# Kernel optimization log

Hardware: AMD Instinct MI355X
Metric: run time of the kernel (lower is better)

Reference implementation:

```python
import jax, jax.numpy as jnp
import numpy as np

MUL_IN = 32      # multiplicity of input 0e irrep (input channels)
MUL_OUT = 32     # multiplicity of each output irrep
NUM_RB = 8       # num_radial_basis
DIAMETER = 5.0
STEPS = (1.0, 1.0, 1.0)
GRID = 32
BATCH = 2
OUT_DIM = MUL_OUT * (1 + 3 + 5)  # 32x0e + 32x1o + 32x2e = 288


def _sus(x):
    # smooth unit step used by e3nn's 'smooth_finite' basis
    return jnp.where(x > 0.0, jnp.exp(-1.0 / jnp.where(x > 0.0, x, 1.0)), 0.0)


def _soft_one_hot(x, start, end, number):
    # e3nn.soft_one_hot_linspace, basis='smooth_finite', start_zero=end_zero=True
    values = jnp.linspace(start, end, number + 2)
    step = values[1] - values[0]
    values = values[1:-1]
    d = (x[..., None] - values) / step
    return 1.14136 * jnp.exp(2.0) * _sus(d + 1.0) * _sus(1.0 - d)


def _lattice():
    r = DIAMETER / 2
    axes = []
    for st in STEPS:
        s = int(np.floor(r / st))
        axes.append(jnp.arange(-s, s + 1.0, dtype=jnp.float32) * st)
    return jnp.stack(jnp.meshgrid(*axes, indexing='ij'), axis=-1)  # [X,Y,Z,3]


def _sph(lattice):
    # e3nn real spherical harmonics (component normalization, normalize=True),
    # e3nn axis/order convention: l=1 -> (y, z, x)
    n = jnp.linalg.norm(lattice, axis=-1, keepdims=True)
    u = lattice / jnp.where(n == 0.0, 1.0, n)
    x, y, z = u[..., 0], u[..., 1], u[..., 2]
    y0 = jnp.ones_like(x)[..., None]
    y1 = jnp.sqrt(3.0) * jnp.stack([y, z, x], axis=-1)
    y2 = jnp.stack([
        jnp.sqrt(15.0) * x * y,
        jnp.sqrt(15.0) * y * z,
        (jnp.sqrt(5.0) / 2.0) * (2.0 * z**2 - x**2 - y**2),
        jnp.sqrt(15.0) * x * z,
        (jnp.sqrt(15.0) / 2.0) * (x**2 - y**2),
    ], axis=-1)
    return [y0, y1, y2]


def _kernel(w0, w1, w2, w_lin):
    lat = _lattice()
    nvox = lat.shape[0] * lat.shape[1] * lat.shape[2]
    emb = _soft_one_hot(jnp.linalg.norm(lat, axis=-1), 0.0, DIAMETER / 2, NUM_RB)
    ys = _sph(lat)
    fan = jnp.sqrt(jnp.asarray(MUL_IN, emb.dtype))  # fully-connected TP path norm
    blocks = []
    for w, y in zip((w0, w1, w2), ys):
        # radial weights per (in-mul u, out-mul v): [X,Y,Z,u,v]
        W = jnp.einsum('xyzk,kuv->xyzuv', emb, w) / nvox
        # scalar-input TP path 0e x l -> l reduces to outer product with Y_lm
        blk = jnp.einsum('xyzuv,xyzm->xyzuvm', W, y) / fan
        blocks.append(blk.reshape(blk.shape[:4] + (-1,)))  # flatten (v, m)
    k = jnp.concatenate(blocks, axis=-1)  # [X,Y,Z,MUL_IN,OUT_DIM]
    # self-connection (FunctionalLinear) replaces the center tap; only 0e->0e path
    center = jnp.concatenate(
        [w_lin / fan, jnp.zeros((MUL_IN, MUL_OUT * (3 + 5)), k.dtype)], axis=-1)
    cx, cy, cz = k.shape[0] // 2, k.shape[1] // 2, k.shape[2] // 2
    return k.at[cx, cy, cz].set(center)


def setup_inputs() -> dict:
    key = jax.random.key(0)
    ks = jax.random.split(key, 5)
    return {
        'x': jax.random.normal(ks[0], (BATCH, GRID, GRID, GRID, MUL_IN), jnp.float32),
        'w0': jax.random.normal(ks[1], (NUM_RB, MUL_IN, MUL_OUT), jnp.float32),
        'w1': jax.random.normal(ks[2], (NUM_RB, MUL_IN, MUL_OUT), jnp.float32),
        'w2': jax.random.normal(ks[3], (NUM_RB, MUL_IN, MUL_OUT), jnp.float32),
        'w_lin': jax.random.normal(ks[4], (MUL_IN, MUL_OUT), jnp.float32),
    }


def reference(x, w0, w1, w2, w_lin):
    k = _kernel(w0, w1, w2, w_lin)  # [5,5,5,32,288]
    return jax.lax.conv_general_dilated(
        x, k, window_strides=(1, 1, 1), padding='SAME',
        dimension_numbers=('NXYZC', 'XYZIO', 'NXYZC'))
```

## Files before the change

kernel.cpp:

```cpp
#include <hip/hip_runtime.h>

typedef __bf16 bf16x8 __attribute__((ext_vector_type(8)));
typedef float f32x4 __attribute__((ext_vector_type(4)));

#define KT_BYTES 2304000
#define NS 18432
#define NV 84

__device__ __forceinline__ unsigned short f2bf(float f) {
    unsigned int u = __builtin_bit_cast(unsigned int, f);
    unsigned int r = (u + 0x7fffu + ((u >> 16) & 1u)) >> 16;
    return (unsigned short)r;
}

__device__ __forceinline__ float sus(float x) {
    return x > 0.0f ? expf(-1.0f / x) : 0.0f;
}

struct VoxTab { int kt[NV]; int xb[NV]; };
constexpr VoxTab mk_tab() {
    VoxTab t{};
    int n = 0;
    for (int dx = 0; dx < 5; dx++)
        for (int dy = 0; dy < 5; dy++)
            for (int dz = 0; dz < 5; dz++) {
                int a = dx - 2, b = dy - 2, c = dz - 2;
                if (a * a + b * b + c * c <= 6) {
                    t.kt[n] = (dx * 25 + dy * 5 + dz) * NS;
                    t.xb[n] = ((dx * 36 + dy) * 36 + dz) * 32;
                    n++;
                }
            }
    for (; n < NV; n++) { t.kt[n] = 0; t.xb[n] = 0; }
    return t;
}
__constant__ VoxTab TAB = mk_tab();

__global__ __launch_bounds__(512) void build_kt(const float* __restrict__ w0,
                                                const float* __restrict__ w1,
                                                const float* __restrict__ w2,
                                                const float* __restrict__ wlin,
                                                unsigned short* __restrict__ kt) {
    __shared__ float lw[24576];
    const int tid = threadIdx.x;
    {
        const float4* s0 = (const float4*)w0;
        const float4* s1 = (const float4*)w1;
        const float4* s2 = (const float4*)w2;
        for (int u = tid; u < 6144; u += 512) {
            int wsel = u >> 11, r = u & 2047;
            float4 v = (wsel == 0 ? s0[r] : (wsel == 1 ? s1[r] : s2[r]));
            ((float4*)lw)[u] = v;
        }
    }
    __syncthreads();

    const int v = blockIdx.x;
    const int dx = v / 25, dy = (v / 5) % 5, dz = v % 5;
    const float lx = (float)(dx - 2), ly = (float)(dy - 2), lz = (float)(dz - 2);
    const float nr = sqrtf(lx * lx + ly * ly + lz * lz);

    float emb[8];
    const float tt = nr * (9.0f / 2.5f);
    const float C = 1.14136f * expf(2.0f);
    #pragma unroll
    for (int j = 1; j <= 8; j++) {
        float d = tt - (float)j;
        emb[j - 1] = C * sus(d + 1.0f) * sus(1.0f - d);
    }

    float ux = 0.f, uy = 0.f, uz = 0.f;
    if (nr > 0.0f) { ux = lx / nr; uy = ly / nr; uz = lz / nr; }
    float Y[9];
    const float s3 = 1.7320508075688772f, s15 = 3.872983346207417f;
    Y[0] = 1.0f;
    Y[1] = s3 * uy; Y[2] = s3 * uz; Y[3] = s3 * ux;
    Y[4] = s15 * ux * uy;
    Y[5] = s15 * uy * uz;
    Y[6] = 1.1180339887498949f * (2.0f * uz * uz - ux * ux - uy * uy);
    Y[7] = s15 * ux * uz;
    Y[8] = 0.5f * s15 * (ux * ux - uy * uy);

    const float rfan = 0.17677669529663687f;

    for (int e = tid; e < 9216; e += 512) {
        const int ci = e / 288, o = e % 288;
        int wsel, co, yi;
        if (o < 32)       { wsel = 0; co = o; yi = 0; }
        else if (o < 128) { int t = o - 32;  wsel = 1; co = t / 3; yi = 1 + t % 3; }
        else              { int t = o - 128; wsel = 2; co = t / 5; yi = 4 + t % 5; }
        const float* w = lw + wsel * 8192;
        float s = 0.0f;
        #pragma unroll
        for (int k = 0; k < 8; k++) s += emb[k] * w[k * 1024 + ci * 32 + co];
        float val = s * (1.0f / 125.0f) * Y[yi] * rfan;
        if (v == 62) val = (o < 32) ? wlin[ci * 32 + o] * rfan : 0.0f;
        int r = o * 64 + ci * 2;
        int rs = r ^ (((r >> 7) & 7) << 4);
        kt[v * 9216 + (rs >> 1)] = f2bf(val);
    }
}

__global__ void pad_x2(const float* __restrict__ x, unsigned short* __restrict__ xb) {
    int u = blockIdx.x * blockDim.x + threadIdx.x;
    if (u >= 373248) return;
    const int ci8 = u & 3;
    int t = u >> 2;
    const int pz = t % 36; t /= 36;
    const int py = t % 36; t /= 36;
    const int px = t % 36; const int nn = t / 36;
    const int gx = px - 2, gy = py - 2, gz = pz - 2;
    uint4 ov = {0u, 0u, 0u, 0u};
    if ((unsigned)gx < 32u && (unsigned)gy < 32u && (unsigned)gz < 32u) {
        const float* src = x + ((((size_t)nn * 32 + gx) * 32 + gy) * 32 + gz) * 32 + ci8 * 8;
        float4 f0 = ((const float4*)src)[0];
        float4 f1 = ((const float4*)src)[1];
        ov.x = (unsigned)f2bf(f0.x) | ((unsigned)f2bf(f0.y) << 16);
        ov.y = (unsigned)f2bf(f0.z) | ((unsigned)f2bf(f0.w) << 16);
        ov.z = (unsigned)f2bf(f1.x) | ((unsigned)f2bf(f1.y) << 16);
        ov.w = (unsigned)f2bf(f1.z) | ((unsigned)f2bf(f1.w) << 16);
    }
    ((uint4*)xb)[u] = ov;
}

__global__ __launch_bounds__(512, 4) void conv_mfma(const unsigned short* __restrict__ xb,
                                                    const unsigned short* __restrict__ kt,
                                                    float* __restrict__ out) {
    __shared__ __align__(16) char lds[4 * NS];
    const int tid = threadIdx.x;
    const int lane = tid & 63;
    const int wv = tid >> 6;
    const int l15 = lane & 15, l16 = lane >> 4;
    const int wm = wv & 3, wn = wv >> 2;
    const int o0 = wn * 144;

    const int b = blockIdx.x;
    const int sw = (b & 7) * 64 + (b >> 3);
    const int nn = sw >> 8;
    const int X0 = 2 * ((sw >> 4) & 15);
    const int Y0 = 2 * (sw & 15);

    const unsigned short* xbase = xb + (size_t)nn * 1492992;

    const int axy = ((X0 + (wm >> 1)) * 36 + (Y0 + (wm & 1))) * 36;
    const int aoff0 = (axy + l15) * 32 + l16 * 8;

    int bbase = (o0 + l15) * 64 + l16 * 16;
    bbase ^= ((bbase >> 7) & 7) << 4;

    auto stageB = [&](int ktByte, int slot) {
        const char* src = (const char*)kt + ktByte + wv * 2304;
        char* dst = lds + slot * NS + wv * 2304;
        __builtin_amdgcn_global_load_lds(
            (const __attribute__((address_space(1))) void*)(src + lane * 16),
            (__attribute__((address_space(3))) void*)dst, 16, 0, 0);
        __builtin_amdgcn_global_load_lds(
            (const __attribute__((address_space(1))) void*)(src + 1024 + lane * 16),
            (__attribute__((address_space(3))) void*)(dst + 1024), 16, 0, 0);
        __builtin_amdgcn_global_load_lds(
            (const __attribute__((address_space(1))) void*)(src + 2048 + lane * 4),
            (__attribute__((address_space(3))) void*)(dst + 2048), 4, 0, 0);
    };

    bf16x8 A0[2], A1[2];
    f32x4 acc[2][9];
    #pragma unroll
    for (int i = 0; i < 2; i++)
        #pragma unroll
        for (int j = 0; j < 9; j++)
            acc[i][j] = (f32x4){0.f, 0.f, 0.f, 0.f};

    auto loadA = [&](bf16x8* A, int xoff) {
        const unsigned short* p = xbase + aoff0 + xoff;
        A[0] = *(const bf16x8*)p;
        A[1] = *(const bf16x8*)(p + 512);
    };

    auto compute = [&](bf16x8* A, int slot) {
        const char* bp = lds + slot * NS + bbase;
        #pragma unroll
        for (int nt = 0; nt < 9; nt++) {
            bf16x8 B = *(const bf16x8*)(bp + nt * 1024);
            acc[0][nt] = __builtin_amdgcn_mfma_f32_16x16x32_bf16(A[0], B, acc[0][nt], 0, 0, 0);
            acc[1][nt] = __builtin_amdgcn_mfma_f32_16x16x32_bf16(A[1], B, acc[1][nt], 0, 0, 0);
        }
    };

    #define PHASE(CUR, NXT, K)                                          \
        asm volatile("s_waitcnt vmcnt(3)" ::: "memory");                \
        __builtin_amdgcn_sched_barrier(0);                              \
        __builtin_amdgcn_s_barrier();                                   \
        __builtin_amdgcn_sched_barrier(0);                              \
        loadA(NXT, TAB.xb[(K) + 1]);                                    \
        stageB(TAB.kt[(K) + 3], ((K) + 3) & 3);                         \
        compute(CUR, (K) & 3);

    stageB(TAB.kt[0], 0);
    stageB(TAB.kt[1], 1);
    stageB(TAB.kt[2], 2);
    loadA(A0, TAB.xb[0]);

    #pragma unroll 1
    for (int g = 0; g < 40; g++) {
        const int k = g * 2;
        PHASE(A0, A1, k + 0)
        PHASE(A1, A0, k + 1)
    }
    PHASE(A0, A1, 80)
    #undef PHASE

    const int x = X0 + (wm >> 1);
    const int y = Y0 + (wm & 1);
    #pragma unroll
    for (int s = 0; s < 2; s++) {
        #pragma unroll
        for (int r = 0; r < 4; r++) {
            int z = s * 16 + l16 * 4 + r;
            size_t base = ((((size_t)nn * 32 + x) * 32 + y) * 32 + z) * 288 + o0 + l15;
            #pragma unroll
            for (int nt = 0; nt < 9; nt++)
                out[base + nt * 16] = acc[s][nt][r];
        }
    }
}

extern "C" void kernel_launch(void* const* d_in, const int* in_sizes, int n_in,
                              void* d_out, int out_size, void* d_ws, size_t ws_size,
                              hipStream_t stream) {
    const float* x    = (const float*)d_in[0];
    const float* w0   = (const float*)d_in[1];
    const float* w1   = (const float*)d_in[2];
    const float* w2   = (const float*)d_in[3];
    const float* wlin = (const float*)d_in[4];
    unsigned short* kt = (unsigned short*)d_ws;
    unsigned short* xb = (unsigned short*)((char*)d_ws + KT_BYTES);
    float* out = (float*)d_out;

    hipLaunchKernelGGL(build_kt, dim3(125), dim3(512), 0, stream, w0, w1, w2, wlin, kt);
    hipLaunchKernelGGL(pad_x2, dim3(1458), dim3(256), 0, stream, x, xb);
    hipLaunchKernelGGL(conv_mfma, dim3(512), dim3(512), 0, stream, xb, kt, out);
}
```

Before: 110.2 us.

## Pipeline two voxel taps per barrier with setprio around MFMA blocks

Restructures the main loop so each barrier-separated phase stages B tiles for two future taps, runs MFMAs for two taps under raised wave priority, then issues A loads for the next pair. This halves the number of barriers and groups memory issue away from compute. It also means all 84 taps are iterated (42 pairs) instead of 81, with the table padded to 86. That may add work or change which taps are included, and the A registers are overwritten only after compute, so A-load latency is exposed at the next wait.

After: 109.0 us (median of 2 runs). Within noise of the previous version (-1.1%).

```diff
diff --git a/kernel.cpp b/kernel.cpp
--- a/kernel.cpp
+++ b/kernel.cpp
@@ -5,7 +5,7 @@
 
 #define KT_BYTES 2304000
 #define NS 18432
-#define NV 84
+#define NVT 86
 
 __device__ __forceinline__ unsigned short f2bf(float f) {
     unsigned int u = __builtin_bit_cast(unsigned int, f);
@@ -17,7 +17,7 @@
     return x > 0.0f ? expf(-1.0f / x) : 0.0f;
 }
 
-struct VoxTab { int kt[NV]; int xb[NV]; };
+struct VoxTab { int kt[NVT]; int xb[NVT]; };
 constexpr VoxTab mk_tab() {
     VoxTab t{};
     int n = 0;
@@ -31,7 +31,7 @@
                     n++;
                 }
             }
-    for (; n < NV; n++) { t.kt[n] = 0; t.xb[n] = 0; }
+    for (; n < NVT; n++) { t.kt[n] = 0; t.xb[n] = 0; }
     return t;
 }
 __constant__ VoxTab TAB = mk_tab();
@@ -186,28 +186,29 @@
         }
     };
 
-    #define PHASE(CUR, NXT, K)                                          \
-        asm volatile("s_waitcnt vmcnt(3)" ::: "memory");                \
-        __builtin_amdgcn_sched_barrier(0);                              \
-        __builtin_amdgcn_s_barrier();                                   \
-        __builtin_amdgcn_sched_barrier(0);                              \
-        loadA(NXT, TAB.xb[(K) + 1]);                                    \
-        stageB(TAB.kt[(K) + 3], ((K) + 3) & 3);                         \
-        compute(CUR, (K) & 3);
-
     stageB(TAB.kt[0], 0);
     stageB(TAB.kt[1], 1);
-    stageB(TAB.kt[2], 2);
     loadA(A0, TAB.xb[0]);
+    loadA(A1, TAB.xb[1]);
 
     #pragma unroll 1
-    for (int g = 0; g < 40; g++) {
-        const int k = g * 2;
-        PHASE(A0, A1, k + 0)
-        PHASE(A1, A0, k + 1)
-    }
-    PHASE(A0, A1, 80)
-    #undef PHASE
+    for (int p = 0; p < 42; p++) {
+        const int k = 2 * p;
+        asm volatile("s_waitcnt vmcnt(4)" ::: "memory");
+        __builtin_amdgcn_sched_barrier(0);
+        __builtin_amdgcn_s_barrier();
+        __builtin_amdgcn_sched_barrier(0);
+        stageB(TAB.kt[k + 2], (k + 2) & 3);
+        stageB(TAB.kt[k + 3], (k + 3) & 3);
+        __builtin_amdgcn_sched_barrier(0);
+        __builtin_amdgcn_s_setprio(1);
+        compute(A0, k & 3);
+        compute(A1, (k + 1) & 3);
+        __builtin_amdgcn_s_setprio(0);
+        __builtin_amdgcn_sched_barrier(0);
+        loadA(A0, TAB.xb[k + 2]);
+        loadA(A1, TAB.xb[k + 3]);
+    }
 
     const int x = X0 + (wm >> 1);
     const int y = Y0 + (wm & 1);
```

## Split conv block into 12 waves and software-pipeline LDS B reads with MFMA

Applied to the files above, without the earlier changes.

The conv kernel grows to 768 threads (12 waves), so each wave covers 96 output columns (6 tiles) instead of 144 (9). The main loop now handles two voxel taps per phase. It double-buffers B fragments in registers, reading one tap's B from LDS while MFMAs run on the previous tap, keeps four A register buffers, and raises wave priority around the MFMA section. The aim is to overlap LDS reads with matrix math and raise wave-level parallelism. The cost is more registers for the fragment buffers, a lower blocks-per-CU target, and a reworked staging and wait-count scheme that has to stay correct across the tap offsets.

Result: slower. 145.1 us (+31.7%).

```diff
diff --git a/kernel.cpp b/kernel.cpp
--- a/kernel.cpp
+++ b/kernel.cpp
@@ -5,7 +5,7 @@
 
 #define KT_BYTES 2304000
 #define NS 18432
-#define NV 84
+#define NVT 88
 
 __device__ __forceinline__ unsigned short f2bf(float f) {
     unsigned int u = __builtin_bit_cast(unsigned int, f);
@@ -17,7 +17,7 @@
     return x > 0.0f ? expf(-1.0f / x) : 0.0f;
 }
 
-struct VoxTab { int kt[NV]; int xb[NV]; };
+struct VoxTab { int kt[NVT]; int xb[NVT]; };
 constexpr VoxTab mk_tab() {
     VoxTab t{};
     int n = 0;
@@ -31,7 +31,7 @@
                     n++;
                 }
             }
-    for (; n < NV; n++) { t.kt[n] = 0; t.xb[n] = 0; }
+    for (; n < NVT; n++) { t.kt[n] = 0; t.xb[n] = 0; }
     return t;
 }
 __constant__ VoxTab TAB = mk_tab();
@@ -123,7 +123,7 @@
     ((uint4*)xb)[u] = ov;
 }
 
-__global__ __launch_bounds__(512, 4) void conv_mfma(const unsigned short* __restrict__ xb,
+__global__ __launch_bounds__(768, 3) void conv_mfma(const unsigned short* __restrict__ xb,
                                                     const unsigned short* __restrict__ kt,
                                                     float* __restrict__ out) {
     __shared__ __align__(16) char lds[4 * NS];
@@ -132,7 +132,7 @@
     const int wv = tid >> 6;
     const int l15 = lane & 15, l16 = lane >> 4;
     const int wm = wv & 3, wn = wv >> 2;
-    const int o0 = wn * 144;
+    const int o0 = wn * 96;
 
     const int b = blockIdx.x;
     const int sw = (b & 7) * 64 + (b >> 3);
@@ -149,64 +149,83 @@
     bbase ^= ((bbase >> 7) & 7) << 4;
 
     auto stageB = [&](int ktByte, int slot) {
-        const char* src = (const char*)kt + ktByte + wv * 2304;
-        char* dst = lds + slot * NS + wv * 2304;
-        __builtin_amdgcn_global_load_lds(
-            (const __attribute__((address_space(1))) void*)(src + lane * 16),
-            (__attribute__((address_space(3))) void*)dst, 16, 0, 0);
-        __builtin_amdgcn_global_load_lds(
-            (const __attribute__((address_space(1))) void*)(src + 1024 + lane * 16),
-            (__attribute__((address_space(3))) void*)(dst + 1024), 16, 0, 0);
-        __builtin_amdgcn_global_load_lds(
-            (const __attribute__((address_space(1))) void*)(src + 2048 + lane * 4),
-            (__attribute__((address_space(3))) void*)(dst + 2048), 4, 0, 0);
-    };
-
-    bf16x8 A0[2], A1[2];
-    f32x4 acc[2][9];
+        if (wv < 9) {
+            const char* src = (const char*)kt + ktByte + wv * 2048 + lane * 16;
+            char* dst = lds + slot * NS + wv * 2048;
+            __builtin_amdgcn_global_load_lds(
+                (const __attribute__((address_space(1))) void*)src,
+                (__attribute__((address_space(3))) void*)dst, 16, 0, 0);
+            __builtin_amdgcn_global_load_lds(
+                (const __attribute__((address_space(1))) void*)(src + 1024),
+                (__attribute__((address_space(3))) void*)(dst + 1024), 16, 0, 0);
+        }
+    };
+
+    bf16x8 A[4][2];
+    bf16x8 X[6], Y[6];
+    f32x4 acc[2][6];
     #pragma unroll
     for (int i = 0; i < 2; i++)
         #pragma unroll
-        for (int j = 0; j < 9; j++)
+        for (int j = 0; j < 6; j++)
             acc[i][j] = (f32x4){0.f, 0.f, 0.f, 0.f};
-
-    auto loadA = [&](bf16x8* A, int xoff) {
+    #pragma unroll
+    for (int j = 0; j < 6; j++) {
+        bf16x8 z;
+        #pragma unroll
+        for (int q = 0; q < 8; q++) z[q] = (__bf16)0.0f;
+        Y[j] = z; X[j] = z;
+    }
+
+    auto loadA = [&](bf16x8 (&As)[2], int xoff) {
         const unsigned short* p = xbase + aoff0 + xoff;
-        A[0] = *(const bf16x8*)p;
-        A[1] = *(const bf16x8*)(p + 512);
-    };
-
-    auto compute = [&](bf16x8* A, int slot) {
+        As[0] = *(const bf16x8*)p;
+        As[1] = *(const bf16x8*)(p + 512);
+    };
+
+    auto rdB = [&](bf16x8 (&B)[6], int slot) {
         const char* bp = lds + slot * NS + bbase;
         #pragma unroll
-        for (int nt = 0; nt < 9; nt++) {
-            bf16x8 B = *(const bf16x8*)(bp + nt * 1024);
-            acc[0][nt] = __builtin_amdgcn_mfma_f32_16x16x32_bf16(A[0], B, acc[0][nt], 0, 0, 0);
-            acc[1][nt] = __builtin_amdgcn_mfma_f32_16x16x32_bf16(A[1], B, acc[1][nt], 0, 0, 0);
-        }
-    };
-
-    #define PHASE(CUR, NXT, K)                                          \
-        asm volatile("s_waitcnt vmcnt(3)" ::: "memory");                \
+        for (int nt = 0; nt < 6; nt++)
+            B[nt] = *(const bf16x8*)(bp + nt * 1024);
+    };
+
+    auto mfma6 = [&](bf16x8 (&As)[2], bf16x8 (&B)[6]) {
+        #pragma unroll
+        for (int nt = 0; nt < 6; nt++) {
+            acc[0][nt] = __builtin_amdgcn_mfma_f32_16x16x32_bf16(As[0], B[nt], acc[0][nt], 0, 0, 0);
+            acc[1][nt] = __builtin_amdgcn_mfma_f32_16x16x32_bf16(As[1], B[nt], acc[1][nt], 0, 0, 0);
+        }
+    };
+
+    #define PHASE(SP, SC, SL1, SL2, RS0, RS1, WS0, WS1, K)              \
+        asm volatile("s_waitcnt vmcnt(4)" ::: "memory");                \
         __builtin_amdgcn_sched_barrier(0);                              \
         __builtin_amdgcn_s_barrier();                                   \
         __builtin_amdgcn_sched_barrier(0);                              \
-        loadA(NXT, TAB.xb[(K) + 1]);                                    \
-        stageB(TAB.kt[(K) + 3], ((K) + 3) & 3);                         \
-        compute(CUR, (K) & 3);
+        stageB(TAB.kt[(K) + 2], WS0);                                   \
+        stageB(TAB.kt[(K) + 3], WS1);                                   \
+        loadA(A[SL1], TAB.xb[(K) + 1]);                                 \
+        loadA(A[SL2], TAB.xb[(K) + 2]);                                 \
+        __builtin_amdgcn_sched_barrier(0);                              \
+        rdB(X, RS0);                                                    \
+        __builtin_amdgcn_s_setprio(1);                                  \
+        mfma6(A[SP], Y);                                                \
+        rdB(Y, RS1);                                                    \
+        mfma6(A[SC], X);                                                \
+        __builtin_amdgcn_s_setprio(0);
 
     stageB(TAB.kt[0], 0);
     stageB(TAB.kt[1], 1);
-    stageB(TAB.kt[2], 2);
-    loadA(A0, TAB.xb[0]);
+    loadA(A[3], TAB.xb[0]);
+    loadA(A[0], TAB.xb[0]);
 
     #pragma unroll 1
-    for (int g = 0; g < 40; g++) {
-        const int k = g * 2;
-        PHASE(A0, A1, k + 0)
-        PHASE(A1, A0, k + 1)
-    }
-    PHASE(A0, A1, 80)
+    for (int g = 0; g < 21; g++) {
+        const int k = 4 * g;
+        PHASE(3, 0, 1, 2, 0, 1, 2, 3, k + 0)
+        PHASE(1, 2, 3, 0, 2, 3, 0, 1, k + 2)
+    }
     #undef PHASE
 
     const int x = X0 + (wm >> 1);
@@ -218,7 +237,7 @@
             int z = s * 16 + l16 * 4 + r;
             size_t base = ((((size_t)nn * 32 + x) * 32 + y) * 32 + z) * 288 + o0 + l15;
             #pragma unroll
-            for (int nt = 0; nt < 9; nt++)
+            for (int nt = 0; nt < 6; nt++)
                 out[base + nt * 16] = acc[s][nt][r];
         }
     }
@@ -238,5 +257,5 @@
 
     hipLaunchKernelGGL(build_kt, dim3(125), dim3(512), 0, stream, w0, w1, w2, wlin, kt);
     hipLaunchKernelGGL(pad_x2, dim3(1458), dim3(256), 0, stream, x, xb);
-    hipLaunchKernelGGL(conv_mfma, dim3(512), dim3(512), 0, stream, xb, kt, out);
-}
+    hipLaunchKernelGGL(conv_mfma, dim3(512), dim3(768), 0, stream, xb, kt, out);
+}
```
